# Optimization experiments

Hardware: AMD Instinct MI355X
Metric: run time of the kernel (lower is better)

Reference implementation:

```python
import jax, jax.numpy as jnp
import numpy as np

EPS_BN = 1e-5
EPS_LN = 1e-5


def _gcn_conv(x, W, b, src, dst, n_nodes):
    # PyG GCNConv: h = x @ W, add self-loops, symmetric deg^{-1/2} normalization,
    # scatter-add over edges, then + bias.
    h = x @ W                                            # [N, out]
    ones = jnp.ones(src.shape[0], dtype=h.dtype)
    deg = jax.ops.segment_sum(ones, dst, num_segments=n_nodes) + 1.0  # +1 for self-loop
    dinv = jax.lax.rsqrt(deg)                            # [N]
    coef = dinv[src] * dinv[dst]                         # [E]
    msg = h[src] * coef[:, None]                         # [E, out] gather + scale
    agg = jax.ops.segment_sum(msg, dst, num_segments=n_nodes)
    agg = agg + h * (dinv * dinv)[:, None]               # self-loop contribution
    return agg + b


def _encode(x, edge_index, W1, b1, bn_gamma, bn_beta, W2, b2, ln_gamma, ln_beta, lin_W, lin_b):
    n = x.shape[0]
    src, dst = edge_index[0], edge_index[1]
    h = _gcn_conv(x, W1, b1, src, dst, n)
    # BatchNorm1d (training mode: batch statistics over nodes, biased var)
    mu = jnp.mean(h, axis=0)
    var = jnp.mean((h - mu) ** 2, axis=0)
    h = (h - mu) * jax.lax.rsqrt(var + EPS_BN) * bn_gamma + bn_beta
    h = jax.nn.relu(h)
    h = _gcn_conv(h, W2, b2, src, dst, n)
    # LayerNorm over feature dim
    mu2 = jnp.mean(h, axis=-1, keepdims=True)
    var2 = jnp.mean((h - mu2) ** 2, axis=-1, keepdims=True)
    h = (h - mu2) * jax.lax.rsqrt(var2 + EPS_LN) * ln_gamma + ln_beta
    h = jax.nn.relu(h)
    return h @ lin_W + lin_b


def setup_inputs() -> dict:
    key = jax.random.key(0)
    ks = jax.random.split(key, 16)
    N, E, EL = 100000, 800000, 200000
    C_in, C_hid, C_out = 128, 256, 128
    inp = {}
    inp["x"] = jax.random.normal(ks[0], (N, C_in), dtype=jnp.float32)
    inp["edge_index"] = jax.random.randint(ks[1], (2, E), 0, N, dtype=jnp.int64)
    inp["edge_label_index"] = jax.random.randint(ks[2], (2, EL), 0, N, dtype=jnp.int64)
    inp["cutoff"] = jnp.zeros((), dtype=jnp.float32)
    s1 = 1.0 / np.sqrt(C_in)
    s2 = 1.0 / np.sqrt(C_hid)
    s3 = 1.0 / np.sqrt(C_out)
    inp["W1"] = jax.random.uniform(ks[3], (C_in, C_hid), jnp.float32, -s1, s1)
    inp["b1"] = jnp.zeros((C_hid,), jnp.float32)
    inp["bn_gamma"] = jnp.ones((C_hid,), jnp.float32)
    inp["bn_beta"] = jnp.zeros((C_hid,), jnp.float32)
    inp["W2"] = jax.random.uniform(ks[4], (C_hid, C_out), jnp.float32, -s2, s2)
    inp["b2"] = jnp.zeros((C_out,), jnp.float32)
    inp["ln_gamma"] = jnp.ones((C_out,), jnp.float32)
    inp["ln_beta"] = jnp.zeros((C_out,), jnp.float32)
    inp["lin_W"] = jax.random.uniform(ks[5], (C_out, C_out), jnp.float32, -s3, s3)
    inp["lin_b"] = jax.random.uniform(ks[6], (C_out,), jnp.float32, -s3, s3)
    return inp


def reference(x, edge_index, edge_label_index, cutoff, W1, b1, bn_gamma, bn_beta, W2, b2, ln_gamma, ln_beta, lin_W, lin_b):
    z = _encode(x, edge_index, W1, b1, bn_gamma, bn_beta, W2, b2, ln_gamma, ln_beta, lin_W, lin_b)
    # decode: per-pair dot product + thresholding
    edge_values = jnp.sum(z[edge_label_index[0]] * z[edge_label_index[1]], axis=-1)  # [EL]
    rounded = jnp.where(edge_values < cutoff, jnp.zeros_like(edge_values), jnp.ones_like(edge_values))
    return edge_values, jax.lax.stop_gradient(rounded)
```

## Files before the change

### kernel.cpp

```cpp
#include <hip/hip_runtime.h>
#include <stdint.h>


#define C_IN  128
#define C_HID 256
#define C_OUT 128
#define SCAN_B 256

typedef __attribute__((ext_vector_type(8))) short bf16x8;
typedef __attribute__((ext_vector_type(4))) float f32x4;

__device__ __forceinline__ short f2bf(float f) {
  union { float f; uint32_t u; } v; v.f = f;
  uint32_t r = v.u + 0x7FFFu + ((v.u >> 16) & 1u);
  return (short)(r >> 16);
}
__device__ __forceinline__ uint32_t pack_bf2(float a, float b) {
  return (uint32_t)(uint16_t)f2bf(a) | ((uint32_t)(uint16_t)f2bf(b) << 16);
}
__device__ __forceinline__ float bflo(uint32_t p) {
  union { uint32_t u; float f; } v; v.u = p << 16; return v.f;
}
__device__ __forceinline__ float bfhi(uint32_t p) {
  union { uint32_t u; float f; } v; v.u = p & 0xffff0000u; return v.f;
}

__device__ __forceinline__ void acc8(float* a, uint4 p, float w) {
  a[0] += bflo(p.x) * w; a[1] += bfhi(p.x) * w;
  a[2] += bflo(p.y) * w; a[3] += bfhi(p.y) * w;
  a[4] += bflo(p.z) * w; a[5] += bfhi(p.z) * w;
  a[6] += bflo(p.w) * w; a[7] += bfhi(p.w) * w;
}

__device__ __forceinline__ void async_cp16(const void* g, void* l) {
  __builtin_amdgcn_global_load_lds((const __attribute__((address_space(1))) void*)g,
                                   (__attribute__((address_space(3))) void*)l, 16, 0, 0);
}


__global__ __launch_bounds__(256) void hist_kernel(const int* __restrict__ dst,
                                                   int* __restrict__ counts, int E) {
  int e = blockIdx.x * 256 + threadIdx.x;
  if (e < E) atomicAdd(&counts[dst[e]], 1);
}

__global__ __launch_bounds__(256) void dinv_kernel(const int* __restrict__ counts,
                                                   float* __restrict__ dinv,
                                                   int* __restrict__ cursor, int N) {
  int n = blockIdx.x * 256 + threadIdx.x;
  if (n < N) {
    dinv[n] = rsqrtf((float)counts[n] + 1.0f);
    cursor[n] = 0;
  }
}


__global__ __launch_bounds__(256) void scan_part(const int* __restrict__ counts,
                                                 int* __restrict__ blockSums,
                                                 int n, int per) {
  __shared__ int ws[4];
  int b = blockIdx.x;
  int start = b * per, end = min(n, start + per);
  int s = 0;
  for (int i = start + threadIdx.x; i < end; i += 256) s += counts[i];
#pragma unroll
  for (int d = 1; d < 64; d <<= 1) s += __shfl_xor(s, d);
  if ((threadIdx.x & 63) == 0) ws[threadIdx.x >> 6] = s;
  __syncthreads();
  if (threadIdx.x == 0) blockSums[b] = ws[0] + ws[1] + ws[2] + ws[3];
}

__global__ __launch_bounds__(256) void scan_bsums(const int* __restrict__ blockSums,
                                                  int* __restrict__ blockOffs, int B) {
  __shared__ int wsum[4];
  int tid = threadIdx.x, lane = tid & 63, wid = tid >> 6;
  int v = (tid < B) ? blockSums[tid] : 0;
  int x = v;
#pragma unroll
  for (int d = 1; d < 64; d <<= 1) {
    int y = __shfl_up(x, d, 64);
    if (lane >= d) x += y;
  }
  if (lane == 63) wsum[wid] = x;
  __syncthreads();
  if (tid == 0) {
    int run = 0;
#pragma unroll
    for (int w = 0; w < 4; ++w) { int t = wsum[w]; wsum[w] = run; run += t; }
  }
  __syncthreads();
  if (tid < B) blockOffs[tid] = wsum[wid] + x - v;
}

__global__ __launch_bounds__(256) void scan_final(const int* __restrict__ counts,
                                                  const int* __restrict__ blockOffs,
                                                  int* __restrict__ row_ptr,
                                                  int n, int per) {
  __shared__ int wsum[4];
  __shared__ int sbase;
  int tid = threadIdx.x, lane = tid & 63, wid = tid >> 6;
  int b = blockIdx.x;
  int start = b * per, end = min(n + 1, start + per);
  if (tid == 0) sbase = blockOffs[b];
  __syncthreads();
  for (int chunk = start; chunk < end; chunk += 256) {
    int idx = chunk + tid;
    int v = (idx < n) ? counts[idx] : 0;
    int x = v;
#pragma unroll
    for (int d = 1; d < 64; d <<= 1) {
      int y = __shfl_up(x, d, 64);
      if (lane >= d) x += y;
    }
    if (lane == 63) wsum[wid] = x;
    __syncthreads();
    if (tid == 0) {
      int run = sbase;
#pragma unroll
      for (int w = 0; w < 4; ++w) { int t = wsum[w]; wsum[w] = run; run += t; }
      sbase = run;
    }
    __syncthreads();
    if (idx < end) row_ptr[idx] = wsum[wid] + x - v;
    __syncthreads();
  }
}

__global__ __launch_bounds__(256) void place_kernel(const int* __restrict__ src,
                                                    const int* __restrict__ dst,
                                                    const int* __restrict__ row_ptr,
                                                    int* __restrict__ cursor,
                                                    const float* __restrict__ dinv,
                                                    int2* __restrict__ edges, int E) {
  int e = blockIdx.x * 256 + threadIdx.x;
  if (e < E) {
    int d = dst[e], s = src[e];
    int pos = row_ptr[d] + atomicAdd(&cursor[d], 1);
    int2 ed; ed.x = s; ed.y = __float_as_int(dinv[s] * dinv[d]);
    edges[pos] = ed;
  }
}


__global__ __launch_bounds__(256) void cvt_bf16_kernel(const float* __restrict__ in,
                                                       short* __restrict__ out, int n4) {
  int i = blockIdx.x * 256 + threadIdx.x;
  if (i >= n4) return;
  float4 v = ((const float4*)in)[i];
  short4 o;
  o.x = f2bf(v.x); o.y = f2bf(v.y); o.z = f2bf(v.z); o.w = f2bf(v.w);
  ((short4*)out)[i] = o;
}

__global__ __launch_bounds__(256) void cvt_wT_kernel(const float* __restrict__ W,
                                                     short* __restrict__ WT, int K, int N) {
  int i = blockIdx.x * 256 + threadIdx.x;
  if (i >= K * N) return;
  int k = i / N, n = i - k * N;
  WT[(size_t)n * K + k] = f2bf(W[i]);
}


template <int MODE>
__global__ __launch_bounds__(256, 2) void bgemm_big(const short* __restrict__ A,
                                                    const short* __restrict__ BT,
                                                    const float* __restrict__ bias,
                                                    void* __restrict__ Cout,
                                                    float* __restrict__ pS,
                                                    float* __restrict__ pSS,
                                                    int M, int N, int K) {
  __shared__ short smem[2 * 128 * 128];
  short* As = smem;
  short* Bs = smem + 128 * 128;
  const int tid = threadIdx.x;
  const int w = tid >> 6, lane = tid & 63;
  const int wM = w >> 1, wN = w & 1;
  const int rowBase = blockIdx.y * 128;
  const int colBase = blockIdx.x * 128;
  const int l15 = lane & 15, q = lane >> 4;

  f32x4 acc[4][4];
#pragma unroll
  for (int i = 0; i < 4; ++i)
#pragma unroll
    for (int j = 0; j < 4; ++j) acc[i][j] = (f32x4){0.f, 0.f, 0.f, 0.f};

  for (int k0 = 0; k0 < K; k0 += 128) {
#pragma unroll
    for (int it = 0; it < 8; ++it) {
      int p = it * 256 + tid;
      int row = p >> 4, kcp = p & 15;
      int kc = kcp ^ (row & 15);
      int gm = rowBase + row; if (gm >= M) gm = M - 1;
      async_cp16(A + (size_t)gm * K + k0 + kc * 8, &As[(it * 256 + w * 64) * 8]);
    }
#pragma unroll
    for (int it = 0; it < 8; ++it) {
      int p = it * 256 + tid;
      int row = p >> 4, kcp = p & 15;
      int kc = kcp ^ (row & 15);
      async_cp16(BT + (size_t)(colBase + row) * K + k0 + kc * 8,
                 &Bs[(it * 256 + w * 64) * 8]);
    }
    __syncthreads();

#pragma unroll
    for (int ks = 0; ks < 4; ++ks) {
      bf16x8 af[4], bfr[4];
#pragma unroll
      for (int tm = 0; tm < 4; ++tm) {
        int row = wM * 64 + tm * 16 + l15;
        int kcp = (ks * 4 + q) ^ l15;
        af[tm] = *(const bf16x8*)&As[(row * 16 + kcp) * 8];
      }
#pragma unroll
      for (int tn = 0; tn < 4; ++tn) {
        int row = wN * 64 + tn * 16 + l15;
        int kcp = (ks * 4 + q) ^ l15;
        bfr[tn] = *(const bf16x8*)&Bs[(row * 16 + kcp) * 8];
      }
#pragma unroll
      for (int tm = 0; tm < 4; ++tm)
#pragma unroll
        for (int tn = 0; tn < 4; ++tn)
          acc[tm][tn] = __builtin_amdgcn_mfma_f32_16x16x32_bf16(af[tm], bfr[tn],
                                                                acc[tm][tn], 0, 0, 0);
    }
    __syncthreads();
  }

  if (MODE == 2) {
#pragma unroll
    for (int tn = 0; tn < 4; ++tn) {
      int col = colBase + wN * 64 + tn * 16 + l15;
      float bv = bias ? bias[col] : 0.0f;
      float s = 0.f, ss = 0.f;
#pragma unroll
      for (int tm = 0; tm < 4; ++tm) {
        int r0 = rowBase + wM * 64 + tm * 16 + q * 4;
#pragma unroll
        for (int r = 0; r < 4; ++r) {
          if (r0 + r < M) { float v = acc[tm][tn][r] + bv; s += v; ss += v * v; }
        }
      }
      s += __shfl_xor(s, 16); s += __shfl_xor(s, 32);
      ss += __shfl_xor(ss, 16); ss += __shfl_xor(ss, 32);
      if (q == 0) {
        int prow = blockIdx.y * 2 + wM;
        pS[(size_t)prow * C_HID + col] = s;
        pSS[(size_t)prow * C_HID + col] = ss;
      }
    }
  }

  if (MODE == 0) {
    float* S = (float*)smem;
#pragma unroll
    for (int tn = 0; tn < 4; ++tn) {
      int col = wN * 64 + tn * 16 + l15;
      float bv = bias ? bias[colBase + col] : 0.0f;
#pragma unroll
      for (int tm = 0; tm < 4; ++tm) {
        int r0 = wM * 64 + tm * 16 + q * 4;
#pragma unroll
        for (int r = 0; r < 4; ++r) S[(r0 + r) * 128 + col] = acc[tm][tn][r] + bv;
      }
    }
    __syncthreads();
    float* Cf = (float*)Cout;
#pragma unroll
    for (int it = 0; it < 16; ++it) {
      int p = it * 256 + tid;
      int row = p >> 5, c = p & 31;
      int gm = rowBase + row;
      if (gm < M)
        *(uint4*)&Cf[(size_t)gm * N + colBase + c * 4] = ((const uint4*)S)[p];
    }
  } else {
    short* S = As;
#pragma unroll
    for (int tn = 0; tn < 4; ++tn) {
      int col = wN * 64 + tn * 16 + l15;
      float bv = bias ? bias[colBase + col] : 0.0f;
#pragma unroll
      for (int tm = 0; tm < 4; ++tm) {
        int r0 = wM * 64 + tm * 16 + q * 4;
#pragma unroll
        for (int r = 0; r < 4; ++r) S[(r0 + r) * 128 + col] = f2bf(acc[tm][tn][r] + bv);
      }
    }
    __syncthreads();
    short* Cb = (short*)Cout;
#pragma unroll
    for (int it = 0; it < 8; ++it) {
      int p = it * 256 + tid;
      int row = p >> 4, c = p & 15;
      int gm = rowBase + row;
      if (gm < M)
        *(uint4*)&Cb[(size_t)gm * N + colBase + c * 8] = ((const uint4*)S)[p];
    }
  }
}


__global__ __launch_bounds__(256) void bn_red1_kernel(const float* __restrict__ pS,
                                                      const float* __restrict__ pSS,
                                                      float* __restrict__ oS,
                                                      float* __restrict__ oSS, int R) {
  int c = threadIdx.x;
  int per = (R + gridDim.x - 1) / gridDim.x;
  int r0 = blockIdx.x * per, r1 = min(R, r0 + per);
  float s = 0.f, ss = 0.f;
  for (int r = r0; r < r1; ++r) {
    s += pS[(size_t)r * C_HID + c];
    ss += pSS[(size_t)r * C_HID + c];
  }
  oS[(size_t)blockIdx.x * C_HID + c] = s;
  oSS[(size_t)blockIdx.x * C_HID + c] = ss;
}

__global__ __launch_bounds__(256) void bn_red2_kernel(const float* __restrict__ oS,
                                                      const float* __restrict__ oSS,
                                                      const float* __restrict__ gamma,
                                                      const float* __restrict__ beta,
                                                      float* __restrict__ bnp,
                                                      int G, float invN) {
  int c = threadIdx.x;
  float s = 0.f, ss = 0.f;
  for (int g = 0; g < G; ++g) {
    s += oS[(size_t)g * C_HID + c];
    ss += oSS[(size_t)g * C_HID + c];
  }
  float mu = s * invN;
  float var = ss * invN - mu * mu;
  float sc = gamma[c] * rsqrtf(var + 1e-5f);
  bnp[c] = sc;
  bnp[C_HID + c] = beta[c] - mu * sc;
}


__global__ __launch_bounds__(256) void bn_apply_kernel(const uint32_t* __restrict__ hb,
                                                       const float* __restrict__ bnp,
                                                       uint32_t* __restrict__ ob,
                                                       int total) {
  int i = blockIdx.x * 256 + threadIdx.x;
  if (i >= total) return;
  int c = (i & 127) * 2;
  float sc0 = bnp[c], sc1 = bnp[c + 1];
  float sh0 = bnp[C_HID + c], sh1 = bnp[C_HID + c + 1];
  uint32_t p = hb[i];
  float o0 = fmaxf(bflo(p) * sc0 + sh0, 0.0f);
  float o1 = fmaxf(bfhi(p) * sc1 + sh1, 0.0f);
  ob[i] = pack_bf2(o0, o1);
}


__global__ __launch_bounds__(256) void agg_x_kernel(const uint4* __restrict__ xb4,
                                                    const float* __restrict__ dinv,
                                                    const int* __restrict__ row_ptr,
                                                    const int2* __restrict__ edges,
                                                    uint4* __restrict__ out4, int N) {
  int g = (blockIdx.x * 256 + threadIdx.x) >> 4;
  int sl = threadIdx.x & 15;
  if (g >= N) return;
  int e0 = row_ptr[g], e1 = row_ptr[g + 1];
  float a[8] = {0.f, 0.f, 0.f, 0.f, 0.f, 0.f, 0.f, 0.f};
  int e = e0;
  for (; e + 4 <= e1; e += 4) {
    int2 ed0 = edges[e], ed1 = edges[e + 1], ed2 = edges[e + 2], ed3 = edges[e + 3];
    uint4 p0 = xb4[(size_t)ed0.x * 16 + sl];
    uint4 p1 = xb4[(size_t)ed1.x * 16 + sl];
    uint4 p2 = xb4[(size_t)ed2.x * 16 + sl];
    uint4 p3 = xb4[(size_t)ed3.x * 16 + sl];
    acc8(a, p0, __int_as_float(ed0.y));
    acc8(a, p1, __int_as_float(ed1.y));
    acc8(a, p2, __int_as_float(ed2.y));
    acc8(a, p3, __int_as_float(ed3.y));
  }
  for (; e < e1; ++e) {
    int2 ed = edges[e];
    uint4 p = xb4[(size_t)ed.x * 16 + sl];
    acc8(a, p, __int_as_float(ed.y));
  }
  float dn = dinv[g];
  uint4 ps = xb4[(size_t)g * 16 + sl];
  acc8(a, ps, dn * dn);
  uint4 o;
  o.x = pack_bf2(a[0], a[1]); o.y = pack_bf2(a[2], a[3]);
  o.z = pack_bf2(a[4], a[5]); o.w = pack_bf2(a[6], a[7]);
  out4[(size_t)g * 16 + sl] = o;
}

__global__ __launch_bounds__(256) void agg_ln_kernel(const uint4* __restrict__ hb4,
                                                     const float* __restrict__ dinv,
                                                     const int* __restrict__ row_ptr,
                                                     const int2* __restrict__ edges,
                                                     const float* __restrict__ bias,
                                                     const float* __restrict__ gamma,
                                                     const float* __restrict__ beta,
                                                     uint4* __restrict__ zb4, int N) {
  int g = (blockIdx.x * 256 + threadIdx.x) >> 4;
  int sl = threadIdx.x & 15;
  if (g >= N) return;
  int e0 = row_ptr[g], e1 = row_ptr[g + 1];
  float a[8] = {0.f, 0.f, 0.f, 0.f, 0.f, 0.f, 0.f, 0.f};
  int e = e0;
  for (; e + 4 <= e1; e += 4) {
    int2 ed0 = edges[e], ed1 = edges[e + 1], ed2 = edges[e + 2], ed3 = edges[e + 3];
    uint4 p0 = hb4[(size_t)ed0.x * 16 + sl];
    uint4 p1 = hb4[(size_t)ed1.x * 16 + sl];
    uint4 p2 = hb4[(size_t)ed2.x * 16 + sl];
    uint4 p3 = hb4[(size_t)ed3.x * 16 + sl];
    acc8(a, p0, __int_as_float(ed0.y));
    acc8(a, p1, __int_as_float(ed1.y));
    acc8(a, p2, __int_as_float(ed2.y));
    acc8(a, p3, __int_as_float(ed3.y));
  }
  for (; e < e1; ++e) {
    int2 ed = edges[e];
    uint4 p = hb4[(size_t)ed.x * 16 + sl];
    acc8(a, p, __int_as_float(ed.y));
  }
  float dn = dinv[g];
  uint4 ps = hb4[(size_t)g * 16 + sl];
  acc8(a, ps, dn * dn);

  int c = sl * 8;
  float4 bv0 = *(const float4*)&bias[c];
  float4 bv1 = *(const float4*)&bias[c + 4];
  a[0] += bv0.x; a[1] += bv0.y; a[2] += bv0.z; a[3] += bv0.w;
  a[4] += bv1.x; a[5] += bv1.y; a[6] += bv1.z; a[7] += bv1.w;

  float s = 0.f, ss = 0.f;
#pragma unroll
  for (int j = 0; j < 8; ++j) { s += a[j]; ss += a[j] * a[j]; }
#pragma unroll
  for (int d = 1; d < 16; d <<= 1) {
    s += __shfl_xor(s, d);
    ss += __shfl_xor(ss, d);
  }
  float mu = s * (1.0f / C_OUT);
  float var = ss * (1.0f / C_OUT) - mu * mu;
  float rs = rsqrtf(var + 1e-5f);
  float4 g0 = *(const float4*)&gamma[c];
  float4 g1 = *(const float4*)&gamma[c + 4];
  float4 t0 = *(const float4*)&beta[c];
  float4 t1 = *(const float4*)&beta[c + 4];
  float o[8];
  o[0] = fmaxf((a[0] - mu) * rs * g0.x + t0.x, 0.0f);
  o[1] = fmaxf((a[1] - mu) * rs * g0.y + t0.y, 0.0f);
  o[2] = fmaxf((a[2] - mu) * rs * g0.z + t0.z, 0.0f);
  o[3] = fmaxf((a[3] - mu) * rs * g0.w + t0.w, 0.0f);
  o[4] = fmaxf((a[4] - mu) * rs * g1.x + t1.x, 0.0f);
  o[5] = fmaxf((a[5] - mu) * rs * g1.y + t1.y, 0.0f);
  o[6] = fmaxf((a[6] - mu) * rs * g1.z + t1.z, 0.0f);
  o[7] = fmaxf((a[7] - mu) * rs * g1.w + t1.w, 0.0f);
  uint4 ov;
  ov.x = pack_bf2(o[0], o[1]); ov.y = pack_bf2(o[2], o[3]);
  ov.z = pack_bf2(o[4], o[5]); ov.w = pack_bf2(o[6], o[7]);
  zb4[(size_t)g * 16 + sl] = ov;
}


__global__ __launch_bounds__(256) void decode_kernel(const float4* __restrict__ z4,
                                                     const int* __restrict__ eli,
                                                     const float* __restrict__ cutoff,
                                                     float* __restrict__ out, int EL) {
  int g = (blockIdx.x * 256 + threadIdx.x) >> 5;
  int sl = threadIdx.x & 31;
  if (g >= EL) return;
  int a = eli[g];
  int b = eli[EL + g];
  float4 va = z4[(size_t)a * 32 + sl];
  float4 vb = z4[(size_t)b * 32 + sl];
  float s = va.x * vb.x + va.y * vb.y + va.z * vb.z + va.w * vb.w;
#pragma unroll
  for (int d = 1; d < 32; d <<= 1) s += __shfl_xor(s, d);
  if (sl == 0) {
    out[g] = s;
    out[EL + g] = (s < cutoff[0]) ? 0.0f : 1.0f;
  }
}


extern "C" void kernel_launch(void* const* d_in, const int* in_sizes, int n_in,
                              void* d_out, int out_size, void* d_ws, size_t ws_size,
                              hipStream_t stream) {
  const float* x        = (const float*)d_in[0];
  const int*   eidx     = (const int*)d_in[1];
  const int*   eli      = (const int*)d_in[2];
  const float* cutoff   = (const float*)d_in[3];
  const float* W1       = (const float*)d_in[4];
  const float* b1       = (const float*)d_in[5];
  const float* bn_gamma = (const float*)d_in[6];
  const float* bn_beta  = (const float*)d_in[7];
  const float* W2       = (const float*)d_in[8];
  const float* b2       = (const float*)d_in[9];
  const float* ln_gamma = (const float*)d_in[10];
  const float* ln_beta  = (const float*)d_in[11];
  const float* lin_W    = (const float*)d_in[12];
  const float* lin_b    = (const float*)d_in[13];
  float* out = (float*)d_out;

  const int N  = in_sizes[0] / C_IN;
  const int E  = in_sizes[1] / 2;
  const int EL = in_sizes[2] / 2;

  const int* src = eidx;
  const int* dst = eidx + E;

  const int MB = (N + 127) / 128;
  const int R  = 2 * MB;

  char* p = (char*)d_ws;
  short* regionA = (short*)p;  p += (size_t)N * 256 * 2;
  short* regionB = (short*)p;  p += (size_t)N * 256 * 2;
  short* h2_bf   = (short*)p;  p += (size_t)N * 128 * 2;
  float* zfin    = (float*)p;  p += (size_t)N * 128 * 4;
  float* dinv    = (float*)p;  p += (size_t)N * 4;
  int* counts    = (int*)p;    p += (size_t)N * 4;
  int* row_ptr   = (int*)p;    p += (size_t)(N + 4) * 4;
  int* cursor    = (int*)p;    p += (size_t)N * 4;
  int2* edges    = (int2*)p;   p += (size_t)E * 8;
  float* pS      = (float*)p;  p += (size_t)R * C_HID * 4;
  float* pSS     = (float*)p;  p += (size_t)R * C_HID * 4;
  float* oS      = (float*)p;  p += 32 * C_HID * 4;
  float* oSS     = (float*)p;  p += 32 * C_HID * 4;
  float* bnp     = (float*)p;  p += 2 * C_HID * 4;
  int* blockSums = (int*)p;    p += SCAN_B * 4;
  int* blockOffs = (int*)p;    p += SCAN_B * 4;
  short* w1t     = (short*)p;  p += (size_t)C_HID * C_IN * 2;
  short* w2t     = (short*)p;  p += (size_t)C_OUT * C_HID * 2;
  short* w3t     = (short*)p;  p += (size_t)C_OUT * C_OUT * 2;

  short* x_bf   = regionA;
  short* xa_bf  = regionA + (size_t)N * 128;
  short* h1_bf  = regionB;
  short* h1n_bf = regionA;
  short* z_bf   = regionB;

  hipMemsetAsync(counts, 0, (size_t)N * 4, stream);

  int eb = (E + 255) / 256;
  int nb = (N + 255) / 256;

  hist_kernel<<<eb, 256, 0, stream>>>(dst, counts, E);
  dinv_kernel<<<nb, 256, 0, stream>>>(counts, dinv, cursor, N);

  int per = (N + 1 + SCAN_B - 1) / SCAN_B;
  scan_part<<<SCAN_B, 256, 0, stream>>>(counts, blockSums, N, per);
  scan_bsums<<<1, 256, 0, stream>>>(blockSums, blockOffs, SCAN_B);
  scan_final<<<SCAN_B, 256, 0, stream>>>(counts, blockOffs, row_ptr, N, per);

  place_kernel<<<eb, 256, 0, stream>>>(src, dst, row_ptr, cursor, dinv, edges, E);

  cvt_wT_kernel<<<(C_IN * C_HID + 255) / 256, 256, 0, stream>>>(W1, w1t, C_IN, C_HID);
  cvt_wT_kernel<<<(C_HID * C_OUT + 255) / 256, 256, 0, stream>>>(W2, w2t, C_HID, C_OUT);
  cvt_wT_kernel<<<(C_OUT * C_OUT + 255) / 256, 256, 0, stream>>>(lin_W, w3t, C_OUT, C_OUT);

  int xn4 = N * C_IN / 4;
  cvt_bf16_kernel<<<(xn4 + 255) / 256, 256, 0, stream>>>(x, x_bf, xn4);

  int gb = ((size_t)N * 16 + 255) / 256;
  agg_x_kernel<<<gb, 256, 0, stream>>>((const uint4*)x_bf, dinv, row_ptr, edges,
                                       (uint4*)xa_bf, N);

  dim3 g1(C_HID / 128, MB);
  bgemm_big<2><<<g1, 256, 0, stream>>>(xa_bf, w1t, b1, h1_bf, pS, pSS, N, C_HID, C_IN);

  bn_red1_kernel<<<32, 256, 0, stream>>>(pS, pSS, oS, oSS, R);
  bn_red2_kernel<<<1, 256, 0, stream>>>(oS, oSS, bn_gamma, bn_beta, bnp, 32,
                                        1.0f / (float)N);

  int bnb = ((size_t)N * 128 + 255) / 256;
  bn_apply_kernel<<<bnb, 256, 0, stream>>>((const uint32_t*)h1_bf, bnp,
                                           (uint32_t*)h1n_bf, N * 128);

  dim3 g2(C_OUT / 128, MB);
  bgemm_big<1><<<g2, 256, 0, stream>>>(h1n_bf, w2t, nullptr, h2_bf, nullptr, nullptr,
                                       N, C_OUT, C_HID);

  agg_ln_kernel<<<gb, 256, 0, stream>>>((const uint4*)h2_bf, dinv, row_ptr, edges,
                                        b2, ln_gamma, ln_beta, (uint4*)z_bf, N);

  dim3 g3(C_OUT / 128, MB);
  bgemm_big<0><<<g3, 256, 0, stream>>>(z_bf, w3t, lin_b, zfin, nullptr, nullptr,
                                       N, C_OUT, C_OUT);

  int db = ((size_t)EL * 32 + 255) / 256;
  decode_kernel<<<db, 256, 0, stream>>>((const float4*)zfin, eli, cutoff, out, EL);
}
```

Before: 431.6 us.

## Fuse BN apply into second GEMM, bf16 final embeddings, record atomic offsets

BatchNorm scale/shift plus ReLU now runs inside the second GEMM's A-tile load, which removes the separate bn_apply pass over the hidden activations. The final linear layer writes bf16 instead of fp32, and decode reads bf16 with 16 lanes per pair, which halves the embedding traffic at some cost in precision. The histogram kernel keeps the atomic return value as each edge's slot, so placing edges into CSR needs no second atomic pass. The three weight conversions are merged into one launch. The fused GEMM load uses synchronous loads plus math instead of async global-to-LDS copies, which may slow that GEMM's main loop.

```diff
diff --git a/kernel.cpp b/kernel.cpp
--- a/kernel.cpp
+++ b/kernel.cpp
@@ -23,6 +23,9 @@
 }
 __device__ __forceinline__ float bfhi(uint32_t p) {
   union { uint32_t u; float f; } v; v.u = p & 0xffff0000u; return v.f;
+}
+__device__ __forceinline__ float bfs(short s) {
+  union { uint32_t u; float f; } v; v.u = ((uint32_t)(uint16_t)s) << 16; return v.f;
 }
 
 __device__ __forceinline__ void acc8(float* a, uint4 p, float w) {
@@ -39,19 +42,16 @@
 
 
 __global__ __launch_bounds__(256) void hist_kernel(const int* __restrict__ dst,
-                                                   int* __restrict__ counts, int E) {
+                                                   int* __restrict__ counts,
+                                                   int* __restrict__ ofs, int E) {
   int e = blockIdx.x * 256 + threadIdx.x;
-  if (e < E) atomicAdd(&counts[dst[e]], 1);
+  if (e < E) ofs[e] = atomicAdd(&counts[dst[e]], 1);
 }
 
 __global__ __launch_bounds__(256) void dinv_kernel(const int* __restrict__ counts,
-                                                   float* __restrict__ dinv,
-                                                   int* __restrict__ cursor, int N) {
+                                                   float* __restrict__ dinv, int N) {
   int n = blockIdx.x * 256 + threadIdx.x;
-  if (n < N) {
-    dinv[n] = rsqrtf((float)counts[n] + 1.0f);
-    cursor[n] = 0;
-  }
+  if (n < N) dinv[n] = rsqrtf((float)counts[n] + 1.0f);
 }
 
 
@@ -129,13 +129,13 @@
 __global__ __launch_bounds__(256) void place_kernel(const int* __restrict__ src,
                                                     const int* __restrict__ dst,
                                                     const int* __restrict__ row_ptr,
-                                                    int* __restrict__ cursor,
+                                                    const int* __restrict__ ofs,
                                                     const float* __restrict__ dinv,
                                                     int2* __restrict__ edges, int E) {
   int e = blockIdx.x * 256 + threadIdx.x;
   if (e < E) {
     int d = dst[e], s = src[e];
-    int pos = row_ptr[d] + atomicAdd(&cursor[d], 1);
+    int pos = row_ptr[d] + ofs[e];
     int2 ed; ed.x = s; ed.y = __float_as_int(dinv[s] * dinv[d]);
     edges[pos] = ed;
   }
@@ -152,12 +152,23 @@
   ((short4*)out)[i] = o;
 }
 
-__global__ __launch_bounds__(256) void cvt_wT_kernel(const float* __restrict__ W,
-                                                     short* __restrict__ WT, int K, int N) {
+__global__ __launch_bounds__(256) void cvt_w_all(const float* __restrict__ W1,
+                                                 short* __restrict__ w1t,
+                                                 const float* __restrict__ W2,
+                                                 short* __restrict__ w2t,
+                                                 const float* __restrict__ W3,
+                                                 short* __restrict__ w3t) {
   int i = blockIdx.x * 256 + threadIdx.x;
-  if (i >= K * N) return;
-  int k = i / N, n = i - k * N;
-  WT[(size_t)n * K + k] = f2bf(W[i]);
+  if (i < 32768) {
+    int k = i >> 8, n = i & 255;
+    w1t[n * 128 + k] = f2bf(W1[i]);
+  } else if (i < 65536) {
+    int j = i - 32768; int k = j >> 7, n = j & 127;
+    w2t[n * 256 + k] = f2bf(W2[j]);
+  } else if (i < 81920) {
+    int j = i - 65536; int k = j >> 7, n = j & 127;
+    w3t[n * 128 + k] = f2bf(W3[j]);
+  }
 }
 
 
@@ -165,9 +176,10 @@
 __global__ __launch_bounds__(256, 2) void bgemm_big(const short* __restrict__ A,
                                                     const short* __restrict__ BT,
                                                     const float* __restrict__ bias,
-                                                    void* __restrict__ Cout,
+                                                    short* __restrict__ Cout,
                                                     float* __restrict__ pS,
                                                     float* __restrict__ pSS,
+                                                    const float* __restrict__ bnp,
                                                     int M, int N, int K) {
   __shared__ short smem[2 * 128 * 128];
   short* As = smem;
@@ -186,13 +198,42 @@
     for (int j = 0; j < 4; ++j) acc[i][j] = (f32x4){0.f, 0.f, 0.f, 0.f};
 
   for (int k0 = 0; k0 < K; k0 += 128) {
-#pragma unroll
-    for (int it = 0; it < 8; ++it) {
-      int p = it * 256 + tid;
-      int row = p >> 4, kcp = p & 15;
-      int kc = kcp ^ (row & 15);
-      int gm = rowBase + row; if (gm >= M) gm = M - 1;
-      async_cp16(A + (size_t)gm * K + k0 + kc * 8, &As[(it * 256 + w * 64) * 8]);
+    if (MODE == 3) {
+#pragma unroll
+      for (int it = 0; it < 8; ++it) {
+        int p = it * 256 + tid;
+        int row = p >> 4, kcp = p & 15;
+        int kc = kcp ^ (row & 15);
+        int gm = rowBase + row; if (gm >= M) gm = M - 1;
+        int c = k0 + kc * 8;
+        bf16x8 av = *(const bf16x8*)&A[(size_t)gm * K + c];
+        float4 s0 = *(const float4*)&bnp[c];
+        float4 s1 = *(const float4*)&bnp[c + 4];
+        float4 h0 = *(const float4*)&bnp[K + c];
+        float4 h1 = *(const float4*)&bnp[K + c + 4];
+        short res[8];
+        res[0] = f2bf(fmaxf(bfs(av[0]) * s0.x + h0.x, 0.f));
+        res[1] = f2bf(fmaxf(bfs(av[1]) * s0.y + h0.y, 0.f));
+        res[2] = f2bf(fmaxf(bfs(av[2]) * s0.z + h0.z, 0.f));
+        res[3] = f2bf(fmaxf(bfs(av[3]) * s0.w + h0.w, 0.f));
+        res[4] = f2bf(fmaxf(bfs(av[4]) * s1.x + h1.x, 0.f));
+        res[5] = f2bf(fmaxf(bfs(av[5]) * s1.y + h1.y, 0.f));
+        res[6] = f2bf(fmaxf(bfs(av[6]) * s1.z + h1.z, 0.f));
+        res[7] = f2bf(fmaxf(bfs(av[7]) * s1.w + h1.w, 0.f));
+        bf16x8 rv;
+#pragma unroll
+        for (int j = 0; j < 8; ++j) rv[j] = res[j];
+        *(bf16x8*)&As[p * 8] = rv;
+      }
+    } else {
+#pragma unroll
+      for (int it = 0; it < 8; ++it) {
+        int p = it * 256 + tid;
+        int row = p >> 4, kcp = p & 15;
+        int kc = kcp ^ (row & 15);
+        int gm = rowBase + row; if (gm >= M) gm = M - 1;
+        async_cp16(A + (size_t)gm * K + k0 + kc * 8, &As[(it * 256 + w * 64) * 8]);
+      }
     }
 #pragma unroll
     for (int it = 0; it < 8; ++it) {
@@ -253,8 +294,8 @@
     }
   }
 
-  if (MODE == 0) {
-    float* S = (float*)smem;
+  {
+    short* S = As;
 #pragma unroll
     for (int tn = 0; tn < 4; ++tn) {
       int col = wN * 64 + tn * 16 + l15;
@@ -263,41 +304,17 @@
       for (int tm = 0; tm < 4; ++tm) {
         int r0 = wM * 64 + tm * 16 + q * 4;
 #pragma unroll
-        for (int r = 0; r < 4; ++r) S[(r0 + r) * 128 + col] = acc[tm][tn][r] + bv;
+        for (int r = 0; r < 4; ++r) S[(r0 + r) * 128 + col] = f2bf(acc[tm][tn][r] + bv);
       }
     }
     __syncthreads();
-    float* Cf = (float*)Cout;
-#pragma unroll
-    for (int it = 0; it < 16; ++it) {
-      int p = it * 256 + tid;
-      int row = p >> 5, c = p & 31;
-      int gm = rowBase + row;
-      if (gm < M)
-        *(uint4*)&Cf[(size_t)gm * N + colBase + c * 4] = ((const uint4*)S)[p];
-    }
-  } else {
-    short* S = As;
-#pragma unroll
-    for (int tn = 0; tn < 4; ++tn) {
-      int col = wN * 64 + tn * 16 + l15;
-      float bv = bias ? bias[colBase + col] : 0.0f;
-#pragma unroll
-      for (int tm = 0; tm < 4; ++tm) {
-        int r0 = wM * 64 + tm * 16 + q * 4;
-#pragma unroll
-        for (int r = 0; r < 4; ++r) S[(r0 + r) * 128 + col] = f2bf(acc[tm][tn][r] + bv);
-      }
-    }
-    __syncthreads();
-    short* Cb = (short*)Cout;
 #pragma unroll
     for (int it = 0; it < 8; ++it) {
       int p = it * 256 + tid;
       int row = p >> 4, c = p & 15;
       int gm = rowBase + row;
       if (gm < M)
-        *(uint4*)&Cb[(size_t)gm * N + colBase + c * 8] = ((const uint4*)S)[p];
+        *(uint4*)&Cout[(size_t)gm * N + colBase + c * 8] = ((const uint4*)S)[p];
     }
   }
 }
@@ -336,22 +353,6 @@
   float sc = gamma[c] * rsqrtf(var + 1e-5f);
   bnp[c] = sc;
   bnp[C_HID + c] = beta[c] - mu * sc;
-}
-
-
-__global__ __launch_bounds__(256) void bn_apply_kernel(const uint32_t* __restrict__ hb,
-                                                       const float* __restrict__ bnp,
-                                                       uint32_t* __restrict__ ob,
-                                                       int total) {
-  int i = blockIdx.x * 256 + threadIdx.x;
-  if (i >= total) return;
-  int c = (i & 127) * 2;
-  float sc0 = bnp[c], sc1 = bnp[c + 1];
-  float sh0 = bnp[C_HID + c], sh1 = bnp[C_HID + c + 1];
-  uint32_t p = hb[i];
-  float o0 = fmaxf(bflo(p) * sc0 + sh0, 0.0f);
-  float o1 = fmaxf(bfhi(p) * sc1 + sh1, 0.0f);
-  ob[i] = pack_bf2(o0, o1);
 }
 
 
@@ -462,20 +463,23 @@
 }
 
 
-__global__ __launch_bounds__(256) void decode_kernel(const float4* __restrict__ z4,
+__global__ __launch_bounds__(256) void decode_kernel(const uint4* __restrict__ zb4,
                                                      const int* __restrict__ eli,
                                                      const float* __restrict__ cutoff,
                                                      float* __restrict__ out, int EL) {
-  int g = (blockIdx.x * 256 + threadIdx.x) >> 5;
-  int sl = threadIdx.x & 31;
+  int g = (blockIdx.x * 256 + threadIdx.x) >> 4;
+  int sl = threadIdx.x & 15;
   if (g >= EL) return;
   int a = eli[g];
   int b = eli[EL + g];
-  float4 va = z4[(size_t)a * 32 + sl];
-  float4 vb = z4[(size_t)b * 32 + sl];
-  float s = va.x * vb.x + va.y * vb.y + va.z * vb.z + va.w * vb.w;
-#pragma unroll
-  for (int d = 1; d < 32; d <<= 1) s += __shfl_xor(s, d);
+  uint4 va = zb4[(size_t)a * 16 + sl];
+  uint4 vb = zb4[(size_t)b * 16 + sl];
+  float s = bflo(va.x) * bflo(vb.x) + bfhi(va.x) * bfhi(vb.x)
+          + bflo(va.y) * bflo(vb.y) + bfhi(va.y) * bfhi(vb.y)
+          + bflo(va.z) * bflo(vb.z) + bfhi(va.z) * bfhi(vb.z)
+          + bflo(va.w) * bflo(vb.w) + bfhi(va.w) * bfhi(vb.w);
+#pragma unroll
+  for (int d = 1; d < 16; d <<= 1) s += __shfl_xor(s, d);
   if (sl == 0) {
     out[g] = s;
     out[EL + g] = (s < cutoff[0]) ? 0.0f : 1.0f;
@@ -516,11 +520,10 @@
   short* regionA = (short*)p;  p += (size_t)N * 256 * 2;
   short* regionB = (short*)p;  p += (size_t)N * 256 * 2;
   short* h2_bf   = (short*)p;  p += (size_t)N * 128 * 2;
-  float* zfin    = (float*)p;  p += (size_t)N * 128 * 4;
   float* dinv    = (float*)p;  p += (size_t)N * 4;
   int* counts    = (int*)p;    p += (size_t)N * 4;
   int* row_ptr   = (int*)p;    p += (size_t)(N + 4) * 4;
-  int* cursor    = (int*)p;    p += (size_t)N * 4;
+  int* ofs       = (int*)p;    p += (size_t)E * 4;
   int2* edges    = (int2*)p;   p += (size_t)E * 8;
   float* pS      = (float*)p;  p += (size_t)R * C_HID * 4;
   float* pSS     = (float*)p;  p += (size_t)R * C_HID * 4;
@@ -536,27 +539,25 @@
   short* x_bf   = regionA;
   short* xa_bf  = regionA + (size_t)N * 128;
   short* h1_bf  = regionB;
-  short* h1n_bf = regionA;
   short* z_bf   = regionB;
+  short* zf_bf  = regionA;
 
   hipMemsetAsync(counts, 0, (size_t)N * 4, stream);
 
   int eb = (E + 255) / 256;
   int nb = (N + 255) / 256;
 
-  hist_kernel<<<eb, 256, 0, stream>>>(dst, counts, E);
-  dinv_kernel<<<nb, 256, 0, stream>>>(counts, dinv, cursor, N);
+  hist_kernel<<<eb, 256, 0, stream>>>(dst, counts, ofs, E);
+  dinv_kernel<<<nb, 256, 0, stream>>>(counts, dinv, N);
 
   int per = (N + 1 + SCAN_B - 1) / SCAN_B;
   scan_part<<<SCAN_B, 256, 0, stream>>>(counts, blockSums, N, per);
   scan_bsums<<<1, 256, 0, stream>>>(blockSums, blockOffs, SCAN_B);
   scan_final<<<SCAN_B, 256, 0, stream>>>(counts, blockOffs, row_ptr, N, per);
 
-  place_kernel<<<eb, 256, 0, stream>>>(src, dst, row_ptr, cursor, dinv, edges, E);
-
-  cvt_wT_kernel<<<(C_IN * C_HID + 255) / 256, 256, 0, stream>>>(W1, w1t, C_IN, C_HID);
-  cvt_wT_kernel<<<(C_HID * C_OUT + 255) / 256, 256, 0, stream>>>(W2, w2t, C_HID, C_OUT);
-  cvt_wT_kernel<<<(C_OUT * C_OUT + 255) / 256, 256, 0, stream>>>(lin_W, w3t, C_OUT, C_OUT);
+  place_kernel<<<eb, 256, 0, stream>>>(src, dst, row_ptr, ofs, dinv, edges, E);
+
+  cvt_w_all<<<320, 256, 0, stream>>>(W1, w1t, W2, w2t, lin_W, w3t);
 
   int xn4 = N * C_IN / 4;
   cvt_bf16_kernel<<<(xn4 + 255) / 256, 256, 0, stream>>>(x, x_bf, xn4);
@@ -566,27 +567,24 @@
                                        (uint4*)xa_bf, N);
 
   dim3 g1(C_HID / 128, MB);
-  bgemm_big<2><<<g1, 256, 0, stream>>>(xa_bf, w1t, b1, h1_bf, pS, pSS, N, C_HID, C_IN);
+  bgemm_big<2><<<g1, 256, 0, stream>>>(xa_bf, w1t, b1, h1_bf, pS, pSS, nullptr,
+                                       N, C_HID, C_IN);
 
   bn_red1_kernel<<<32, 256, 0, stream>>>(pS, pSS, oS, oSS, R);
   bn_red2_kernel<<<1, 256, 0, stream>>>(oS, oSS, bn_gamma, bn_beta, bnp, 32,
                                         1.0f / (float)N);
 
-  int bnb = ((size_t)N * 128 + 255) / 256;
-  bn_apply_kernel<<<bnb, 256, 0, stream>>>((const uint32_t*)h1_bf, bnp,
-                                           (uint32_t*)h1n_bf, N * 128);
-
   dim3 g2(C_OUT / 128, MB);
-  bgemm_big<1><<<g2, 256, 0, stream>>>(h1n_bf, w2t, nullptr, h2_bf, nullptr, nullptr,
-                                       N, C_OUT, C_HID);
+  bgemm_big<3><<<g2, 256, 0, stream>>>(h1_bf, w2t, nullptr, h2_bf, nullptr, nullptr,
+                                       bnp, N, C_OUT, C_HID);
 
   agg_ln_kernel<<<gb, 256, 0, stream>>>((const uint4*)h2_bf, dinv, row_ptr, edges,
                                         b2, ln_gamma, ln_beta, (uint4*)z_bf, N);
 
   dim3 g3(C_OUT / 128, MB);
-  bgemm_big<0><<<g3, 256, 0, stream>>>(z_bf, w3t, lin_b, zfin, nullptr, nullptr,
-                                       N, C_OUT, C_OUT);
-
-  int db = ((size_t)EL * 32 + 255) / 256;
-  decode_kernel<<<db, 256, 0, stream>>>((const float4*)zfin, eli, cutoff, out, EL);
-}
+  bgemm_big<1><<<g3, 256, 0, stream>>>(z_bf, w3t, lin_b, zf_bf, nullptr, nullptr,
+                                       nullptr, N, C_OUT, C_OUT);
+
+  int db = ((size_t)EL * 16 + 255) / 256;
+  decode_kernel<<<db, 256, 0, stream>>>((const uint4*)zf_bf, eli, cutoff, out, EL);
+}
```

New measurement: 369.4 us. 14.4% less time.
